# Performance work log

Measured on AMD Instinct MI355X. Metric: run time of the kernel, lower is better.

The kernel has to match this reference:

```python
import jax, jax.numpy as jnp
import numpy as np

N_NODES = 8192
N_EDGES = 524288
N_PAIRS = 262144
N_TYPES = 86


def _gcn_conv(x, W, b, src, dst, n):
    # PyG GCNConv: transform, add self-loops, symmetric degree normalization,
    # scatter-add aggregation at destination nodes.
    xw = x @ W  # [N, F_out]
    loop = jnp.arange(n, dtype=src.dtype)
    s = jnp.concatenate([src, loop])
    d = jnp.concatenate([dst, loop])
    deg = jax.ops.segment_sum(jnp.ones(d.shape, xw.dtype), d, num_segments=n)
    dinv = jnp.where(deg > 0, jax.lax.rsqrt(deg), 0.0)  # deg^{-1/2}, 0 for isolated
    coef = dinv[s] * dinv[d]  # [E+N]
    out = jax.ops.segment_sum(xw[s] * coef[:, None], d, num_segments=n)
    return out + b


def setup_inputs() -> dict:
    key = jax.random.key(0)
    ks = jax.random.split(key, 10)
    x = jax.random.normal(ks[0], (N_NODES, N_NODES), dtype=jnp.float32)
    edge_index = jax.random.randint(ks[1], (2, N_EDGES), 0, N_NODES, dtype=jnp.int32)
    drug1_idx = jax.random.randint(ks[2], (N_PAIRS,), 0, N_NODES, dtype=jnp.int32)
    drug2_idx = jax.random.randint(ks[3], (N_PAIRS,), 0, N_NODES, dtype=jnp.int32)
    W1 = jax.random.normal(ks[4], (N_NODES, 128), dtype=jnp.float32) / np.sqrt(N_NODES)
    b1 = jnp.zeros((128,), jnp.float32)
    W2 = jax.random.normal(ks[5], (128, 64), dtype=jnp.float32) / np.sqrt(128.0)
    b2 = jnp.zeros((64,), jnp.float32)
    Wfc = jax.random.normal(ks[6], (128, N_TYPES), dtype=jnp.float32) / np.sqrt(128.0)
    bfc = jnp.zeros((N_TYPES,), jnp.float32)
    return {"x": x, "edge_index": edge_index, "drug1_idx": drug1_idx,
            "drug2_idx": drug2_idx, "W1": W1, "b1": b1, "W2": W2, "b2": b2,
            "Wfc": Wfc, "bfc": bfc}


def reference(x, edge_index, drug1_idx, drug2_idx, W1, b1, W2, b2, Wfc, bfc):
    n = x.shape[0]
    src, dst = edge_index[0], edge_index[1]
    h = jax.nn.relu(_gcn_conv(x, W1, b1, src, dst, n))
    # dropout p=0.3 is identity at inference (training=False)
    h = jax.nn.relu(_gcn_conv(h, W2, b2, src, dst, n))
    combined = jnp.concatenate([h[drug1_idx], h[drug2_idx]], axis=1)  # [P, 128]
    return jax.nn.sigmoid(combined @ Wfc + bfc)
```

## Files before the change

### kernel.cpp

```cpp
#include <hip/hip_runtime.h>
#include <math.h>
#include <stdint.h>
#include <stddef.h>

#define N_NODES 8192
#define N_EDGES 524288
#define N_PAIRS 262144
#define N_TYPES 86
#define F1 128
#define F2 64

typedef unsigned short ushort_t;
typedef unsigned int uint_t;
typedef __attribute__((ext_vector_type(8))) short bfrag;
typedef __attribute__((ext_vector_type(4))) float ffrag;

typedef __attribute__((address_space(3))) char lds_char;
typedef __attribute__((address_space(1))) const char g_char;

__device__ __forceinline__ void gload16(const void* g, void* l) {
  __builtin_amdgcn_global_load_lds((const g_char*)g, (lds_char*)l, 16, 0, 0);
}

__device__ inline ushort_t f2bf(float f) {
  uint_t u = __float_as_uint(f);
  uint_t r = u + 0x7fffu + ((u >> 16) & 1u);
  return (ushort_t)(r >> 16);
}
__device__ inline float bf2f(ushort_t h) {
  return __uint_as_float(((uint_t)h) << 16);
}


__global__ void count_deg_k(const int* __restrict__ dst, int* __restrict__ cnt) {
  int e = blockIdx.x * blockDim.x + threadIdx.x;
  if (e < N_EDGES) atomicAdd(&cnt[dst[e]], 1);
}

__global__ void dinv_k(const int* __restrict__ cnt, float* __restrict__ dinv) {
  int i = blockIdx.x * blockDim.x + threadIdx.x;
  if (i < N_NODES) dinv[i] = 1.0f / sqrtf((float)(cnt[i] + 1));
}

__global__ void scan_k(const int* __restrict__ cnt, int* __restrict__ rp,
                       int* __restrict__ fill) {
  __shared__ int s[1024];
  int t = threadIdx.x;
  int v[8];
  int sum = 0;
#pragma unroll
  for (int i = 0; i < 8; i++) { v[i] = cnt[t * 8 + i]; sum += v[i]; }
  s[t] = sum;
  __syncthreads();
  for (int off = 1; off < 1024; off <<= 1) {
    int add = (t >= off) ? s[t - off] : 0;
    __syncthreads();
    s[t] += add;
    __syncthreads();
  }
  int excl = s[t] - sum;
#pragma unroll
  for (int i = 0; i < 8; i++) {
    rp[t * 8 + i] = excl;
    fill[t * 8 + i] = excl;
    excl += v[i];
  }
  if (t == 1023) rp[N_NODES] = excl;
}

__global__ void scatter_k(const int* __restrict__ src, const int* __restrict__ dst,
                          int* fill, int* __restrict__ csr) {
  int e = blockIdx.x * blockDim.x + threadIdx.x;
  if (e < N_EDGES) {
    int d = dst[e];
    int pos = atomicAdd(&fill[d], 1);
    csr[pos] = src[e];
  }
}


__global__ __launch_bounds__(256) void w1split_k(const float* __restrict__ W1,
                                                 ushort_t* __restrict__ W1th,
                                                 ushort_t* __restrict__ W1tl) {
  __shared__ ushort_t lh[32 * 65];
  __shared__ ushort_t ll[32 * 65];
  int tid = threadIdx.x;
  int k0 = blockIdx.x * 64;
  int n0 = blockIdx.y * 32;
#pragma unroll
  for (int i = 0; i < 8; i++) {
    int c = tid + 256 * i;
    int kr = c >> 5, nc = c & 31;
    float v = W1[(size_t)(k0 + kr) * F1 + n0 + nc];
    ushort_t h = f2bf(v);
    ushort_t l = f2bf(v - bf2f(h));
    lh[nc * 65 + kr] = h;
    ll[nc * 65 + kr] = l;
  }
  __syncthreads();
#pragma unroll
  for (int i = 0; i < 2; i++) {
    int c = tid + 256 * i;
    int buf = c >> 8;
    int cc = c & 255;
    int nr = cc >> 3, kc = cc & 7;
    const ushort_t* l = buf ? ll : lh;
    uint4 u;
    u.x = (uint_t)l[nr * 65 + kc * 8 + 0] | ((uint_t)l[nr * 65 + kc * 8 + 1] << 16);
    u.y = (uint_t)l[nr * 65 + kc * 8 + 2] | ((uint_t)l[nr * 65 + kc * 8 + 3] << 16);
    u.z = (uint_t)l[nr * 65 + kc * 8 + 4] | ((uint_t)l[nr * 65 + kc * 8 + 5] << 16);
    u.w = (uint_t)l[nr * 65 + kc * 8 + 6] | ((uint_t)l[nr * 65 + kc * 8 + 7] << 16);
    ushort_t* dst = (buf ? W1tl : W1th) + (size_t)(n0 + nr) * N_NODES + k0 + kc * 8;
    *(uint4*)dst = u;
  }
}


#define BUFSZ 65536
#define OA_H 0
#define OA_L 16384
#define OB_H 32768
#define OB_L 49152

__global__ __launch_bounds__(512) void gemm1_mfma_k(const float* __restrict__ x,
                                                    const ushort_t* __restrict__ W1th,
                                                    const ushort_t* __restrict__ W1tl,
                                                    float* __restrict__ part, int kspan) {
  __shared__ __align__(16) char lds[2 * BUFSZ];
  int tid = threadIdx.x;
  int m_blk = blockIdx.x * 128;
  int kbase = blockIdx.y * kspan;
  int ktiles = kspan >> 6;
  int wave = tid >> 6, lane = tid & 63;
  int wr = wave >> 2, wc = wave & 3;
  int lrow = lane & 15, kgrp = lane >> 4;
  int xr = (lrow & 7) << 4;
  int kb0 = kgrp * 16;

  const ushort_t* bsrc = (wave < 4) ? W1th : W1tl;
  int b_quarter = (wave & 3) * 4096;
  int ob = (wave < 4) ? OB_H : OB_L;
  int brow_g = (wave & 3) * 32 + (lane >> 3);
  int kel = (((lane & 7) ^ ((lane >> 3) & 7)) << 3);

  ffrag acc[4][2];
#pragma unroll
  for (int mi = 0; mi < 4; mi++)
#pragma unroll
    for (int ni = 0; ni < 2; ni++) acc[mi][ni] = (ffrag)(0.0f);

  float4 av[4];

#define LOADA(K0)                                                                    \
  {                                                                                  \
    _Pragma("unroll") for (int i = 0; i < 4; i++) {                                  \
      int c = tid + 512 * i;                                                         \
      int row = c >> 4, c4 = c & 15;                                                 \
      av[i] = *(const float4*)&x[(size_t)(m_blk + row) * N_NODES + (K0) + 4 * c4];   \
    }                                                                                \
  }

#define LOADB(K0, BUFP)                                                              \
  {                                                                                  \
    _Pragma("unroll") for (int i = 0; i < 4; i++) {                                  \
      const ushort_t* gp = bsrc + (size_t)(brow_g + i * 8) * N_NODES + (K0) + kel;   \
      gload16(gp, (BUFP) + ob + b_quarter + i * 1024);                               \
    }                                                                                \
  }

#define STOREA(BUFP)                                                                 \
  {                                                                                  \
    _Pragma("unroll") for (int i = 0; i < 4; i++) {                                  \
      int c = tid + 512 * i;                                                         \
      int row = c >> 4, c4 = c & 15;                                                 \
      float f0 = av[i].x, f1 = av[i].y, f2 = av[i].z, f3 = av[i].w;                  \
      ushort_t h0 = f2bf(f0), h1 = f2bf(f1), h2 = f2bf(f2), h3 = f2bf(f3);           \
      ushort_t l0 = f2bf(f0 - bf2f(h0)), l1 = f2bf(f1 - bf2f(h1));                   \
      ushort_t l2 = f2bf(f2 - bf2f(h2)), l3 = f2bf(f3 - bf2f(h3));                   \
      uint2 hp, lp;                                                                  \
      hp.x = (uint_t)h0 | ((uint_t)h1 << 16); hp.y = (uint_t)h2 | ((uint_t)h3 << 16);\
      lp.x = (uint_t)l0 | ((uint_t)l1 << 16); lp.y = (uint_t)l2 | ((uint_t)l3 << 16);\
      uint_t off = row * 128 + ((c4 * 8) ^ ((row & 7) << 4));                        \
      *(uint2*)((BUFP) + OA_H + off) = hp;                                           \
      *(uint2*)((BUFP) + OA_L + off) = lp;                                           \
    }                                                                                \
  }

#define COMPUTE(BUFP)                                                                \
  {                                                                                  \
    _Pragma("unroll") for (int ks = 0; ks < 2; ++ks) {                               \
      int cb = ks * 64 + kb0;                                                        \
      bfrag bh[2], bl[2];                                                            \
      _Pragma("unroll") for (int ni = 0; ni < 2; ni++) {                             \
        int brow = wc * 32 + ni * 16 + lrow;                                         \
        uint_t boff = brow * 128 + (cb ^ xr);                                        \
        bh[ni] = *(const bfrag*)((BUFP) + OB_H + boff);                              \
        bl[ni] = *(const bfrag*)((BUFP) + OB_L + boff);                              \
      }                                                                              \
      _Pragma("unroll") for (int mi = 0; mi < 4; mi++) {                             \
        int arow = wr * 64 + mi * 16 + lrow;                                         \
        uint_t aoff = arow * 128 + (cb ^ xr);                                        \
        bfrag ah = *(const bfrag*)((BUFP) + OA_H + aoff);                            \
        bfrag al = *(const bfrag*)((BUFP) + OA_L + aoff);                            \
        _Pragma("unroll") for (int ni = 0; ni < 2; ni++) {                           \
          acc[mi][ni] = __builtin_amdgcn_mfma_f32_16x16x32_bf16(ah, bh[ni], acc[mi][ni], 0, 0, 0); \
          acc[mi][ni] = __builtin_amdgcn_mfma_f32_16x16x32_bf16(ah, bl[ni], acc[mi][ni], 0, 0, 0); \
          acc[mi][ni] = __builtin_amdgcn_mfma_f32_16x16x32_bf16(al, bh[ni], acc[mi][ni], 0, 0, 0); \
        }                                                                            \
      }                                                                              \
    }                                                                                \
  }

  LOADA(kbase);
  LOADB(kbase, lds);
  STOREA(lds);
  __syncthreads();

  int cur = 0;
  for (int kt = 0; kt < ktiles - 1; ++kt) {
    char* bufC = lds + cur * BUFSZ;
    char* bufN = lds + (cur ^ 1) * BUFSZ;
    int k0n = kbase + ((kt + 1) << 6);
    LOADA(k0n);
    LOADB(k0n, bufN);
    __builtin_amdgcn_sched_barrier(0);
    COMPUTE(bufC);
    STOREA(bufN);
    __syncthreads();
    cur ^= 1;
  }
  COMPUTE(lds + cur * BUFSZ);

  float* outp = part + (size_t)blockIdx.y * (N_NODES * F1);
#pragma unroll
  for (int mi = 0; mi < 4; mi++) {
#pragma unroll
    for (int ni = 0; ni < 2; ni++) {
      int col = wc * 32 + ni * 16 + lrow;
#pragma unroll
      for (int r = 0; r < 4; r++) {
        int row = m_blk + wr * 64 + mi * 16 + kgrp * 4 + r;
        outp[(size_t)row * F1 + col] = acc[mi][ni][r];
      }
    }
  }
#undef LOADA
#undef LOADB
#undef STOREA
#undef COMPUTE
}

__global__ void reduceS_k(const float* __restrict__ part, float* __restrict__ xw1, int S) {
  int i = blockIdx.x * blockDim.x + threadIdx.x;
  float4 a = ((const float4*)part)[i];
  for (int s = 1; s < S; s++) {
    float4 b = ((const float4*)(part + (size_t)s * N_NODES * F1))[i];
    a.x += b.x; a.y += b.y; a.z += b.z; a.w += b.w;
  }
  ((float4*)xw1)[i] = a;
}


template <int F>
__global__ void agg_k(const float* __restrict__ xw, const int* __restrict__ csr,
                      const int* __restrict__ rp, const float* __restrict__ dinv,
                      const float* __restrict__ bias, float* __restrict__ hout) {
  int node = blockIdx.x;
  int f = threadIdx.x;
  __shared__ int sidx[F];
  __shared__ float sdv[F];
  int beg = rp[node], end = rp[node + 1];
  float acc = 0.f;
  for (int base = beg; base < end; base += F) {
    int n = end - base;
    if (n > F) n = F;
    __syncthreads();
    if (f < n) {
      int s = csr[base + f];
      sidx[f] = s;
      sdv[f] = dinv[s];
    }
    __syncthreads();
    for (int i = 0; i < n; i++) acc += xw[(size_t)sidx[i] * F + f] * sdv[i];
  }
  float dv = dinv[node];
  float v = (acc + xw[(size_t)node * F + f] * dv) * dv + bias[f];
  hout[(size_t)node * F + f] = v > 0.f ? v : 0.f;
}


__global__ __launch_bounds__(256) void gemm2_k(const float* __restrict__ h1,
                                               const float* __restrict__ W2,
                                               float* __restrict__ xw2) {
  __shared__ float W2s[F1 * F2];
  __shared__ float As[16 * F1];
  int tid = threadIdx.x;
  int r0 = blockIdx.x * 16;
#pragma unroll
  for (int j = 0; j < 8; j++)
    ((float4*)W2s)[tid + 256 * j] = ((const float4*)W2)[tid + 256 * j];
#pragma unroll
  for (int j = 0; j < 2; j++)
    ((float4*)As)[tid + 256 * j] = ((const float4*)(h1 + (size_t)r0 * F1))[tid + 256 * j];
  __syncthreads();
  int r = tid >> 4, c4 = tid & 15;
  float4 acc = make_float4(0.f, 0.f, 0.f, 0.f);
#pragma unroll 8
  for (int k = 0; k < F1; k++) {
    float a = As[r * F1 + k];
    float4 bv = *(float4*)&W2s[k * F2 + 4 * c4];
    acc.x += a * bv.x; acc.y += a * bv.y; acc.z += a * bv.z; acc.w += a * bv.w;
  }
  *(float4*)&xw2[(size_t)(r0 + r) * F2 + 4 * c4] = acc;
}


__global__ void pboth_k(const float* __restrict__ h2, const float* __restrict__ Wfc,
                        float* __restrict__ P) {
  __shared__ float hs[64 * 16];
  int tid = threadIdx.x;
  int r0 = blockIdx.x * 16;
  for (int idx = tid; idx < 256; idx += 192) {
    int row = idx >> 4, k4 = idx & 15;
    float4 h = *(const float4*)&h2[(size_t)(r0 + row) * F2 + 4 * k4];
    hs[(4 * k4 + 0) * 16 + row] = h.x;
    hs[(4 * k4 + 1) * 16 + row] = h.y;
    hs[(4 * k4 + 2) * 16 + row] = h.z;
    hs[(4 * k4 + 3) * 16 + row] = h.w;
  }
  __syncthreads();
  if (tid < 172) {
    int half = tid < 86 ? 0 : 1;
    int j = tid - 86 * half;
    const float* wp = Wfc + (size_t)(64 * half) * N_TYPES + j;
    float acc[16];
#pragma unroll
    for (int r = 0; r < 16; r++) acc[r] = 0.f;
    for (int k = 0; k < 64; k++) {
      float w = wp[(size_t)k * N_TYPES];
      const float* hk = &hs[k * 16];
#pragma unroll
      for (int r = 0; r < 16; r++) acc[r] += hk[r] * w;
    }
#pragma unroll
    for (int r = 0; r < 16; r++) P[(size_t)(r0 + r) * 172 + tid] = acc[r];
  }
}


__global__ void final_k(const float* __restrict__ P, const int* __restrict__ d1,
                        const int* __restrict__ d2, const float* __restrict__ bfc,
                        float* __restrict__ out) {
  int gid = blockIdx.x * blockDim.x + threadIdx.x;
  if (gid >= N_PAIRS * 43) return;
  int p = gid / 43;
  int j = gid - p * 43;
  int a = d1[p], b = d2[p];
  float2 v1 = *(const float2*)&P[(size_t)a * 172 + 2 * j];
  float2 v2 = *(const float2*)&P[(size_t)b * 172 + 86 + 2 * j];
  float2 bb = *(const float2*)&bfc[2 * j];
  float z0 = v1.x + v2.x + bb.x;
  float z1 = v1.y + v2.y + bb.y;
  float2 o;
  o.x = 1.0f / (1.0f + expf(-z0));
  o.y = 1.0f / (1.0f + expf(-z1));
  *(float2*)&out[(size_t)p * 86 + 2 * j] = o;
}


extern "C" void kernel_launch(void* const* d_in, const int* in_sizes, int n_in,
                              void* d_out, int out_size, void* d_ws, size_t ws_size,
                              hipStream_t stream) {
  const float* x   = (const float*)d_in[0];
  const int*   ei  = (const int*)d_in[1];
  const int*   d1  = (const int*)d_in[2];
  const int*   d2  = (const int*)d_in[3];
  const float* W1  = (const float*)d_in[4];
  const float* b1  = (const float*)d_in[5];
  const float* W2  = (const float*)d_in[6];
  const float* b2  = (const float*)d_in[7];
  const float* Wfc = (const float*)d_in[8];
  const float* bfc = (const float*)d_in[9];
  float* out = (float*)d_out;

  const int* esrc = ei;
  const int* edst = ei + N_EDGES;

  char* w = (char*)d_ws;
  size_t off = 0;
  auto alloc = [&](size_t bytes) -> char* {
    char* p = w + off;
    off += (bytes + 255) & ~(size_t)255;
    return p;
  };
  int*      cnt  = (int*)alloc((size_t)N_NODES * 4);
  float*    dinv = (float*)alloc((size_t)N_NODES * 4);
  int*      rp   = (int*)alloc((size_t)(N_NODES + 1) * 4);
  int*      fill = (int*)alloc((size_t)N_NODES * 4);
  int*      csr  = (int*)alloc((size_t)N_EDGES * 4);
  ushort_t* W1th = (ushort_t*)alloc((size_t)N_NODES * F1 * 2);
  ushort_t* W1tl = (ushort_t*)alloc((size_t)N_NODES * F1 * 2);
  float*    h1   = (float*)alloc((size_t)N_NODES * F1 * 4);
  float*    xw2  = (float*)alloc((size_t)N_NODES * F2 * 4);
  float*    h2   = (float*)alloc((size_t)N_NODES * F2 * 4);
  float*    P    = (float*)alloc((size_t)N_NODES * 172 * 4);

  size_t partBytes = (size_t)N_NODES * F1 * 4;
  int S = 4;
  while (S > 1 && off + (size_t)S * partBytes > ws_size) S >>= 1;
  float* part = (float*)alloc((size_t)S * partBytes);
  float* xw1 = part;
  if (off > ws_size) return;

  hipMemsetAsync(cnt, 0, (size_t)N_NODES * 4, stream);
  count_deg_k<<<N_EDGES / 256, 256, 0, stream>>>(edst, cnt);
  dinv_k<<<N_NODES / 256, 256, 0, stream>>>(cnt, dinv);
  scan_k<<<1, 1024, 0, stream>>>(cnt, rp, fill);
  scatter_k<<<N_EDGES / 256, 256, 0, stream>>>(esrc, edst, fill, csr);

  w1split_k<<<dim3(N_NODES / 64, F1 / 32), 256, 0, stream>>>(W1, W1th, W1tl);
  gemm1_mfma_k<<<dim3(N_NODES / 128, S), 512, 0, stream>>>(x, W1th, W1tl, part, N_NODES / S);
  if (S > 1)
    reduceS_k<<<(N_NODES * F1 / 4) / 256, 256, 0, stream>>>(part, xw1, S);
  agg_k<F1><<<N_NODES, F1, 0, stream>>>(xw1, csr, rp, dinv, b1, h1);

  gemm2_k<<<N_NODES / 16, 256, 0, stream>>>(h1, W2, xw2);
  agg_k<F2><<<N_NODES, F2, 0, stream>>>(xw2, csr, rp, dinv, b2, h2);

  pboth_k<<<N_NODES / 16, 192, 0, stream>>>(h2, Wfc, P);
  final_k<<<(N_PAIRS * 43) / 256, 256, 0, stream>>>(P, d1, d2, bfc, out);
}
```

Before: 267.7 us.

## Restructure gemm1 into 64-row tiles with fine-grained software-pipelined loads

Rewrites the x@W1 MFMA GEMM to use 64-row M tiles with split-K of 2. A 256-wide A window is staged in LDS, B is double-buffered in 32-wide k steps, and loads for the next step are issued before compute under explicit vmcnt waits, barriers and setprio. This is meant to hide the memory latency of streaming the large fp32 x matrix better than the old coarse two-buffer loop, at the cost of 160KB LDS per block, and it hardcodes S=2 and a 4096-wide K span. It also folds the dinv computation into the scan kernel and replaces the memset with a small zeroing kernel to cut launch overhead.

```diff
diff --git a/kernel.cpp b/kernel.cpp
--- a/kernel.cpp
+++ b/kernel.cpp
@@ -32,24 +32,27 @@
 }
 
 
+__global__ void zero_k(int* __restrict__ p) {
+  p[blockIdx.x * 256 + threadIdx.x] = 0;
+}
+
 __global__ void count_deg_k(const int* __restrict__ dst, int* __restrict__ cnt) {
   int e = blockIdx.x * blockDim.x + threadIdx.x;
   if (e < N_EDGES) atomicAdd(&cnt[dst[e]], 1);
 }
 
-__global__ void dinv_k(const int* __restrict__ cnt, float* __restrict__ dinv) {
-  int i = blockIdx.x * blockDim.x + threadIdx.x;
-  if (i < N_NODES) dinv[i] = 1.0f / sqrtf((float)(cnt[i] + 1));
-}
-
 __global__ void scan_k(const int* __restrict__ cnt, int* __restrict__ rp,
-                       int* __restrict__ fill) {
+                       int* __restrict__ fill, float* __restrict__ dinv) {
   __shared__ int s[1024];
   int t = threadIdx.x;
   int v[8];
   int sum = 0;
 #pragma unroll
-  for (int i = 0; i < 8; i++) { v[i] = cnt[t * 8 + i]; sum += v[i]; }
+  for (int i = 0; i < 8; i++) {
+    v[i] = cnt[t * 8 + i];
+    dinv[t * 8 + i] = 1.0f / sqrtf((float)(v[i] + 1));
+    sum += v[i];
+  }
   s[t] = sum;
   __syncthreads();
   for (int off = 1; off < 1024; off <<= 1) {
@@ -116,137 +119,163 @@
 }
 
 
-#define BUFSZ 65536
-#define OA_H 0
-#define OA_L 16384
-#define OB_H 32768
-#define OB_L 49152
+#define AWB(b) ((b) * 65536)
+#define BBB(b) (131072 + (b) * 16384)
+
+#define SCHED0 __builtin_amdgcn_sched_barrier(0)
+#define WAITVM(N)  do { asm volatile("s_waitcnt vmcnt(" #N ")" ::: "memory"); SCHED0; } while (0)
+#define WAITVML(N) do { asm volatile("s_waitcnt vmcnt(" #N ") lgkmcnt(0)" ::: "memory"); SCHED0; } while (0)
 
 __global__ __launch_bounds__(512) void gemm1_mfma_k(const float* __restrict__ x,
                                                     const ushort_t* __restrict__ W1th,
                                                     const ushort_t* __restrict__ W1tl,
-                                                    float* __restrict__ part, int kspan) {
-  __shared__ __align__(16) char lds[2 * BUFSZ];
+                                                    float* __restrict__ part) {
+  __shared__ __align__(16) char lds[163840];
   int tid = threadIdx.x;
-  int m_blk = blockIdx.x * 128;
-  int kbase = blockIdx.y * kspan;
-  int ktiles = kspan >> 6;
   int wave = tid >> 6, lane = tid & 63;
   int wr = wave >> 2, wc = wave & 3;
   int lrow = lane & 15, kgrp = lane >> 4;
-  int xr = (lrow & 7) << 4;
-  int kb0 = kgrp * 16;
+  int m_blk = blockIdx.y * 64;
+  int kbase = blockIdx.x * 4096;
 
   const ushort_t* bsrc = (wave < 4) ? W1th : W1tl;
-  int b_quarter = (wave & 3) * 4096;
-  int ob = (wave < 4) ? OB_H : OB_L;
-  int brow_g = (wave & 3) * 32 + (lane >> 3);
-  int kel = (((lane & 7) ^ ((lane >> 3) & 7)) << 3);
-
-  ffrag acc[4][2];
-#pragma unroll
-  for (int mi = 0; mi < 4; mi++)
+  int b_half = (wave < 4) ? 0 : 8192;
+  int bq = wave & 3;
+  int b_row = bq * 32 + (lane >> 2);
+  int b_kel = ((lane & 3) ^ ((lane >> 2) & 3)) << 3;
+
+  ffrag acc[2][2];
+#pragma unroll
+  for (int mi = 0; mi < 2; mi++)
 #pragma unroll
     for (int ni = 0; ni < 2; ni++) acc[mi][ni] = (ffrag)(0.0f);
 
-  float4 av[4];
-
-#define LOADA(K0)                                                                    \
+  float4 ch[3];
+
+#define ISSUE_B(K0, BSEL)                                                            \
   {                                                                                  \
-    _Pragma("unroll") for (int i = 0; i < 4; i++) {                                  \
-      int c = tid + 512 * i;                                                         \
-      int row = c >> 4, c4 = c & 15;                                                 \
-      av[i] = *(const float4*)&x[(size_t)(m_blk + row) * N_NODES + (K0) + 4 * c4];   \
+    _Pragma("unroll") for (int i = 0; i < 2; i++) {                                  \
+      const ushort_t* gp = bsrc + (size_t)(b_row + i * 16) * N_NODES + (K0) + b_kel; \
+      gload16(gp, lds + BBB(BSEL) + b_half + bq * 2048 + i * 1024);                  \
     }                                                                                \
   }
 
-#define LOADB(K0, BUFP)                                                              \
+#define ISSUE_A(J, KW)                                                               \
+  ch[(J) % 3] = *(const float4*)&x[(size_t)(m_blk + wave * 8 + (J)) * N_NODES + (KW) + lane * 4];
+
+#define CONV_A(J, BSEL)                                                              \
   {                                                                                  \
-    _Pragma("unroll") for (int i = 0; i < 4; i++) {                                  \
-      const ushort_t* gp = bsrc + (size_t)(brow_g + i * 8) * N_NODES + (K0) + kel;   \
-      gload16(gp, (BUFP) + ob + b_quarter + i * 1024);                               \
+    float4 v = ch[(J) % 3];                                                          \
+    int r = wave * 8 + (J);                                                          \
+    ushort_t h0 = f2bf(v.x), h1 = f2bf(v.y), h2 = f2bf(v.z), h3 = f2bf(v.w);         \
+    ushort_t l0 = f2bf(v.x - bf2f(h0)), l1 = f2bf(v.y - bf2f(h1));                   \
+    ushort_t l2 = f2bf(v.z - bf2f(h2)), l3 = f2bf(v.w - bf2f(h3));                   \
+    uint2 hp, lp;                                                                    \
+    hp.x = (uint_t)h0 | ((uint_t)h1 << 16); hp.y = (uint_t)h2 | ((uint_t)h3 << 16);  \
+    lp.x = (uint_t)l0 | ((uint_t)l1 << 16); lp.y = (uint_t)l2 | ((uint_t)l3 << 16);  \
+    uint_t off = r * 512 + ((((lane >> 1) ^ (r & 15))) << 4) + ((lane & 1) << 3);    \
+    *(uint2*)(lds + AWB(BSEL) + off) = hp;                                           \
+    *(uint2*)(lds + AWB(BSEL) + 32768 + off) = lp;                                   \
+  }
+
+#define COMPUTE(S, ASEL)                                                             \
+  {                                                                                  \
+    bfrag bh[2], bl[2];                                                              \
+    _Pragma("unroll") for (int ni = 0; ni < 2; ni++) {                               \
+      int brow = wc * 32 + ni * 16 + lrow;                                           \
+      uint_t boff = brow * 64 + ((kgrp * 16) ^ ((brow & 3) << 4));                   \
+      bh[ni] = *(const bfrag*)(lds + BBB((S) & 1) + boff);                           \
+      bl[ni] = *(const bfrag*)(lds + BBB((S) & 1) + 8192 + boff);                    \
     }                                                                                \
-  }
-
-#define STOREA(BUFP)                                                                 \
-  {                                                                                  \
-    _Pragma("unroll") for (int i = 0; i < 4; i++) {                                  \
-      int c = tid + 512 * i;                                                         \
-      int row = c >> 4, c4 = c & 15;                                                 \
-      float f0 = av[i].x, f1 = av[i].y, f2 = av[i].z, f3 = av[i].w;                  \
-      ushort_t h0 = f2bf(f0), h1 = f2bf(f1), h2 = f2bf(f2), h3 = f2bf(f3);           \
-      ushort_t l0 = f2bf(f0 - bf2f(h0)), l1 = f2bf(f1 - bf2f(h1));                   \
-      ushort_t l2 = f2bf(f2 - bf2f(h2)), l3 = f2bf(f3 - bf2f(h3));                   \
-      uint2 hp, lp;                                                                  \
-      hp.x = (uint_t)h0 | ((uint_t)h1 << 16); hp.y = (uint_t)h2 | ((uint_t)h3 << 16);\
-      lp.x = (uint_t)l0 | ((uint_t)l1 << 16); lp.y = (uint_t)l2 | ((uint_t)l3 << 16);\
-      uint_t off = row * 128 + ((c4 * 8) ^ ((row & 7) << 4));                        \
-      *(uint2*)((BUFP) + OA_H + off) = hp;                                           \
-      *(uint2*)((BUFP) + OA_L + off) = lp;                                           \
-    }                                                                                \
-  }
-
-#define COMPUTE(BUFP)                                                                \
-  {                                                                                  \
-    _Pragma("unroll") for (int ks = 0; ks < 2; ++ks) {                               \
-      int cb = ks * 64 + kb0;                                                        \
-      bfrag bh[2], bl[2];                                                            \
+    _Pragma("unroll") for (int mi = 0; mi < 2; mi++) {                               \
+      int arow = wr * 32 + mi * 16 + lrow;                                           \
+      uint_t aoff = arow * 512 + ((((S) * 4 + kgrp) ^ (arow & 15)) << 4);            \
+      bfrag ah = *(const bfrag*)(lds + AWB(ASEL) + aoff);                            \
+      bfrag al = *(const bfrag*)(lds + AWB(ASEL) + 32768 + aoff);                    \
       _Pragma("unroll") for (int ni = 0; ni < 2; ni++) {                             \
-        int brow = wc * 32 + ni * 16 + lrow;                                         \
-        uint_t boff = brow * 128 + (cb ^ xr);                                        \
-        bh[ni] = *(const bfrag*)((BUFP) + OB_H + boff);                              \
-        bl[ni] = *(const bfrag*)((BUFP) + OB_L + boff);                              \
-      }                                                                              \
-      _Pragma("unroll") for (int mi = 0; mi < 4; mi++) {                             \
-        int arow = wr * 64 + mi * 16 + lrow;                                         \
-        uint_t aoff = arow * 128 + (cb ^ xr);                                        \
-        bfrag ah = *(const bfrag*)((BUFP) + OA_H + aoff);                            \
-        bfrag al = *(const bfrag*)((BUFP) + OA_L + aoff);                            \
-        _Pragma("unroll") for (int ni = 0; ni < 2; ni++) {                           \
-          acc[mi][ni] = __builtin_amdgcn_mfma_f32_16x16x32_bf16(ah, bh[ni], acc[mi][ni], 0, 0, 0); \
-          acc[mi][ni] = __builtin_amdgcn_mfma_f32_16x16x32_bf16(ah, bl[ni], acc[mi][ni], 0, 0, 0); \
-          acc[mi][ni] = __builtin_amdgcn_mfma_f32_16x16x32_bf16(al, bh[ni], acc[mi][ni], 0, 0, 0); \
-        }                                                                            \
+        acc[mi][ni] = __builtin_amdgcn_mfma_f32_16x16x32_bf16(ah, bh[ni], acc[mi][ni], 0, 0, 0); \
+        acc[mi][ni] = __builtin_amdgcn_mfma_f32_16x16x32_bf16(ah, bl[ni], acc[mi][ni], 0, 0, 0); \
+        acc[mi][ni] = __builtin_amdgcn_mfma_f32_16x16x32_bf16(al, bh[ni], acc[mi][ni], 0, 0, 0); \
       }                                                                              \
     }                                                                                \
   }
 
-  LOADA(kbase);
-  LOADB(kbase, lds);
-  STOREA(lds);
-  __syncthreads();
-
-  int cur = 0;
-  for (int kt = 0; kt < ktiles - 1; ++kt) {
-    char* bufC = lds + cur * BUFSZ;
-    char* bufN = lds + (cur ^ 1) * BUFSZ;
-    int k0n = kbase + ((kt + 1) << 6);
-    LOADA(k0n);
-    LOADB(k0n, bufN);
-    __builtin_amdgcn_sched_barrier(0);
-    COMPUTE(bufC);
-    STOREA(bufN);
-    __syncthreads();
-    cur ^= 1;
-  }
-  COMPUTE(lds + cur * BUFSZ);
-
-  float* outp = part + (size_t)blockIdx.y * (N_NODES * F1);
-#pragma unroll
-  for (int mi = 0; mi < 4; mi++) {
+  ISSUE_B(kbase, 0);
+  SCHED0;
+  {
+    float4 ch8[8];
+#pragma unroll
+    for (int j = 0; j < 8; j++)
+      ch8[j] = *(const float4*)&x[(size_t)(m_blk + wave * 8 + j) * N_NODES + kbase + lane * 4];
+    WAITVML(0);
+#pragma unroll
+    for (int j = 0; j < 8; j++) {
+      float4 v = ch8[j];
+      int r = wave * 8 + j;
+      ushort_t h0 = f2bf(v.x), h1 = f2bf(v.y), h2 = f2bf(v.z), h3 = f2bf(v.w);
+      ushort_t l0 = f2bf(v.x - bf2f(h0)), l1 = f2bf(v.y - bf2f(h1));
+      ushort_t l2 = f2bf(v.z - bf2f(h2)), l3 = f2bf(v.w - bf2f(h3));
+      uint2 hp, lp;
+      hp.x = (uint_t)h0 | ((uint_t)h1 << 16); hp.y = (uint_t)h2 | ((uint_t)h3 << 16);
+      lp.x = (uint_t)l0 | ((uint_t)l1 << 16); lp.y = (uint_t)l2 | ((uint_t)l3 << 16);
+      uint_t off = r * 512 + ((((lane >> 1) ^ (r & 15))) << 4) + ((lane & 1) << 3);
+      *(uint2*)(lds + AWB(0) + off) = hp;
+      *(uint2*)(lds + AWB(0) + 32768 + off) = lp;
+    }
+  }
+  asm volatile("s_waitcnt lgkmcnt(0)" ::: "memory");
+  SCHED0;
+  __builtin_amdgcn_s_barrier();
+  SCHED0;
+
+  for (int w = 0; w < 16; ++w) {
+    const int awc = w & 1, awn = (w + 1) & 1;
+    const int wns = (w < 15) ? (w + 1) : 15;
+    const int kw = kbase + w * 256;
+    const int kwn = kbase + wns * 256;
+#pragma unroll
+    for (int s = 0; s < 8; ++s) {
+      int kbn = (s < 7) ? (kw + (s + 1) * 32) : kwn;
+      ISSUE_B(kbn, (s + 1) & 1);
+      SCHED0;
+      if (s == 0) { ISSUE_A(0, kwn); ISSUE_A(1, kwn); }
+      else if (s < 7) { ISSUE_A(s + 1, kwn); }
+      SCHED0;
+      __builtin_amdgcn_s_setprio(1);
+      COMPUTE(s, awc);
+      __builtin_amdgcn_s_setprio(0);
+      if (s >= 1 && s <= 6) {
+        WAITVM(3);
+        CONV_A(s - 1, awn);
+      } else if (s == 7) {
+        WAITVM(2);
+        CONV_A(6, awn);
+        CONV_A(7, awn);
+      }
+      if (s == 0) { WAITVML(2); }
+      else if (s < 7) { WAITVML(1); }
+      else { WAITVML(0); }
+      __builtin_amdgcn_s_barrier();
+      SCHED0;
+    }
+  }
+
+  float* outp = part + (size_t)blockIdx.x * (N_NODES * F1);
+#pragma unroll
+  for (int mi = 0; mi < 2; mi++) {
 #pragma unroll
     for (int ni = 0; ni < 2; ni++) {
       int col = wc * 32 + ni * 16 + lrow;
 #pragma unroll
       for (int r = 0; r < 4; r++) {
-        int row = m_blk + wr * 64 + mi * 16 + kgrp * 4 + r;
+        int row = m_blk + wr * 32 + mi * 16 + kgrp * 4 + r;
         outp[(size_t)row * F1 + col] = acc[mi][ni][r];
       }
     }
   }
-#undef LOADA
-#undef LOADB
-#undef STOREA
+#undef ISSUE_B
+#undef ISSUE_A
+#undef CONV_A
 #undef COMPUTE
 }
 
@@ -405,28 +434,25 @@
   float*    h2   = (float*)alloc((size_t)N_NODES * F2 * 4);
   float*    P    = (float*)alloc((size_t)N_NODES * 172 * 4);
 
+  const int S = 2;
   size_t partBytes = (size_t)N_NODES * F1 * 4;
-  int S = 4;
-  while (S > 1 && off + (size_t)S * partBytes > ws_size) S >>= 1;
   float* part = (float*)alloc((size_t)S * partBytes);
   float* xw1 = part;
   if (off > ws_size) return;
 
-  hipMemsetAsync(cnt, 0, (size_t)N_NODES * 4, stream);
+  zero_k<<<N_NODES / 256, 256, 0, stream>>>(cnt);
   count_deg_k<<<N_EDGES / 256, 256, 0, stream>>>(edst, cnt);
-  dinv_k<<<N_NODES / 256, 256, 0, stream>>>(cnt, dinv);
-  scan_k<<<1, 1024, 0, stream>>>(cnt, rp, fill);
+  scan_k<<<1, 1024, 0, stream>>>(cnt, rp, fill, dinv);
   scatter_k<<<N_EDGES / 256, 256, 0, stream>>>(esrc, edst, fill, csr);
 
   w1split_k<<<dim3(N_NODES / 64, F1 / 32), 256, 0, stream>>>(W1, W1th, W1tl);
-  gemm1_mfma_k<<<dim3(N_NODES / 128, S), 512, 0, stream>>>(x, W1th, W1tl, part, N_NODES / S);
-  if (S > 1)
-    reduceS_k<<<(N_NODES * F1 / 4) / 256, 256, 0, stream>>>(part, xw1, S);
+  gemm1_mfma_k<<<dim3(S, N_NODES / 64), 512, 0, stream>>>(x, W1th, W1tl, part);
+  reduceS_k<<<(N_NODES * F1 / 4) / 256, 256, 0, stream>>>(part, xw1, S);
   agg_k<F1><<<N_NODES, F1, 0, stream>>>(xw1, csr, rp, dinv, b1, h1);
 
   gemm2_k<<<N_NODES / 16, 256, 0, stream>>>(h1, W2, xw2);
   agg_k<F2><<<N_NODES, F2, 0, stream>>>(xw2, csr, rp, dinv, b2, h2);
 
   pboth_k<<<N_NODES / 16, 192, 0, stream>>>(h2, Wfc, P);
-  final_k<<<(N_PAIRS * 43) / 256, 256, 0, stream>>>(P, d1, d2, bfc, out);
-}
+  final_k<<<(N_PAIRS * 43 + 255) / 256, 256, 0, stream>>>(P, d1, d2, bfc, out);
+}
```

Result: slower. 293.7 us (+9.7%).
